# Kernel tuning notes

Measured on AMD Instinct MI355X. Metric: run time of the kernel, lower is better.

Reference implementation:

```python
import jax, jax.numpy as jnp
import numpy as np

TAU = 0.07
EPS_NORM = 1e-8


def setup_inputs() -> dict:
    key = jax.random.key(0)
    k1, k2 = jax.random.split(key)
    N, D = 8192, 128
    feats = jax.random.normal(k1, (N, D), dtype=jnp.float32)
    labels = jax.random.randint(k2, (N,), 0, 512, dtype=jnp.int64)
    return {"feats": feats, "labels": labels}


def _l2n(x, eps=EPS_NORM):
    # F.normalize: x / max(||x||_2, eps)
    n = jnp.sqrt(jnp.sum(x * x, axis=-1, keepdims=True))
    return x / jnp.maximum(n, eps)


def reference(feats, labels):
    N = feats.shape[0]
    f = _l2n(feats)
    sim = (f @ f.T) / TAU                       # [N, N]
    eye = jnp.eye(N, dtype=sim.dtype)
    logits = sim - eye * 1e9                    # suppress self-similarity
    pos_mask = (labels[:, None] == labels[None, :]) & (~jnp.eye(N, dtype=bool))
    exp_logits = jnp.exp(logits)                # [N, N]
    numer = jnp.sum(exp_logits * pos_mask, axis=1)
    denom = jnp.maximum(jnp.sum(exp_logits, axis=1), 1e-8)
    valid = jnp.sum(pos_mask, axis=1) > 0
    loss = -jnp.log((numer + 1e-12) / denom)    # [N]
    n_valid = jnp.sum(valid)
    mean_loss = jnp.sum(jnp.where(valid, loss, 0.0)) / jnp.maximum(n_valid, 1)
    return jnp.where(n_valid > 0, mean_loss, 0.0)
```

## Files before the change

### kernel.cpp

```cpp
#include <hip/hip_runtime.h>
#include <hip/hip_bf16.h>

#define N_ROWS 8192
#define DIM 128
#define IBLK 128

#define SQRT_SC 4.539816f
#define LN2F 0.6931471805599453f

typedef __attribute__((ext_vector_type(8))) short bf16x8;
typedef __attribute__((ext_vector_type(4))) float f32x4;

__global__ __launch_bounds__(256) void normalize_kernel(
    const float* __restrict__ feats, __hip_bfloat16* __restrict__ nf) {
  int wid = threadIdx.x >> 6;
  int lane = threadIdx.x & 63;
  int row = blockIdx.x * 4 + wid;
  const float* rp = feats + (size_t)row * DIM;
  float2 v = *reinterpret_cast<const float2*>(rp + lane * 2);
  float ss = v.x * v.x + v.y * v.y;
  #pragma unroll
  for (int m = 1; m < 64; m <<= 1) ss += __shfl_xor(ss, m, 64);
  float scale = SQRT_SC / fmaxf(sqrtf(ss), 1e-8f);
  __hip_bfloat162 h2;
  h2.x = __float2bfloat16(v.x * scale);
  h2.y = __float2bfloat16(v.y * scale);
  *reinterpret_cast<__hip_bfloat162*>(nf + (size_t)row * DIM + lane * 2) = h2;
}

__global__ __launch_bounds__(256) void supcon_main(
    const __hip_bfloat16* __restrict__ nf, const int* __restrict__ labels,
    float* __restrict__ denomP, float* __restrict__ numerP, int jrange) {
  const ushort* F = reinterpret_cast<const ushort*>(nf);
  int lane = threadIdx.x & 63;
  int wid = threadIdx.x >> 6;
  int col = lane & 15;
  int kg = lane >> 4;
  int ibase = blockIdx.x * IBLK + wid * 32;
  int jbase = blockIdx.y * jrange;

  bf16x8 a[2][4];
  int labi[2][4];
  #pragma unroll
  for (int it = 0; it < 2; ++it) {
    const ushort* ap = F + (size_t)(ibase + it * 16 + col) * DIM + kg * 8;
    #pragma unroll
    for (int c = 0; c < 4; ++c)
      a[it][c] = *reinterpret_cast<const bf16x8*>(ap + c * 32);
    #pragma unroll
    for (int r = 0; r < 4; ++r)
      labi[it][r] = labels[ibase + it * 16 + kg * 4 + r];
  }
  float denom[2][4] = {}, numer[2][4] = {};

  const ushort* bp = F + (size_t)(jbase + col) * DIM + kg * 8;
  const int* lp = labels + jbase + col;
  int ntiles = jrange >> 4;
  for (int jt = 0; jt < ntiles; ++jt) {
    int jb = jbase + (jt << 4);
    int labj = *lp;
    bf16x8 b[4];
    #pragma unroll
    for (int c = 0; c < 4; ++c)
      b[c] = *reinterpret_cast<const bf16x8*>(bp + c * 32);
    f32x4 d[2];
    #pragma unroll
    for (int it = 0; it < 2; ++it) {
      f32x4 acc = {0.f, 0.f, 0.f, 0.f};
      #pragma unroll
      for (int c = 0; c < 4; ++c)
        acc = __builtin_amdgcn_mfma_f32_16x16x32_bf16(a[it][c], b[c], acc,
                                                      0, 0, 0);
      d[it] = acc;
    }
    if (jb + 16 > ibase && jb < ibase + 32) {
      int gj = jb + col;
      #pragma unroll
      for (int it = 0; it < 2; ++it)
        #pragma unroll
        for (int r = 0; r < 4; ++r) {
          float e = __builtin_amdgcn_exp2f(d[it][r]);
          if (ibase + it * 16 + kg * 4 + r == gj) e = 0.f;
          denom[it][r] += e;
          numer[it][r] += (labi[it][r] == labj) ? e : 0.f;
        }
    } else {
      #pragma unroll
      for (int it = 0; it < 2; ++it)
        #pragma unroll
        for (int r = 0; r < 4; ++r) {
          float e = __builtin_amdgcn_exp2f(d[it][r]);
          denom[it][r] += e;
          numer[it][r] += (labi[it][r] == labj) ? e : 0.f;
        }
    }
    bp += (size_t)16 * DIM;
    lp += 16;
  }

  #pragma unroll
  for (int m = 1; m < 16; m <<= 1)
    #pragma unroll
    for (int it = 0; it < 2; ++it)
      #pragma unroll
      for (int r = 0; r < 4; ++r) {
        denom[it][r] += __shfl_xor(denom[it][r], m, 64);
        numer[it][r] += __shfl_xor(numer[it][r], m, 64);
      }
  if (col == 0) {
    size_t s = blockIdx.y;
    #pragma unroll
    for (int it = 0; it < 2; ++it)
      #pragma unroll
      for (int r = 0; r < 4; ++r) {
        size_t idx = s * N_ROWS + (ibase + it * 16 + kg * 4 + r);
        denomP[idx] = denom[it][r];
        numerP[idx] = numer[it][r];
      }
  }
}

__global__ __launch_bounds__(256) void finalize1(
    const float* __restrict__ denomP, const float* __restrict__ numerP,
    const int* __restrict__ labels, float* __restrict__ blkP, int jsplit) {
  __shared__ int hist[512];
  int tid = threadIdx.x;
  for (int i = tid; i < 512; i += 256) hist[i] = 0;
  __syncthreads();
  for (int i = tid; i < N_ROWS; i += 256) atomicAdd(&hist[labels[i]], 1);
  __syncthreads();

  int row = blockIdx.x * 256 + tid;
  float den = 0.f, num = 0.f;
  for (int s = 0; s < jsplit; ++s) {
    den += denomP[(size_t)s * N_ROWS + row];
    num += numerP[(size_t)s * N_ROWS + row];
  }
  bool valid = (hist[labels[row]] - 1) > 0;
  float loss = LN2F * (__builtin_amdgcn_logf(fmaxf(den, 1e-8f)) -
                       __builtin_amdgcn_logf(num + 1e-12f));
  float ls = valid ? loss : 0.f;
  float lc = valid ? 1.f : 0.f;
  #pragma unroll
  for (int m = 1; m < 64; m <<= 1) {
    ls += __shfl_xor(ls, m, 64);
    lc += __shfl_xor(lc, m, 64);
  }
  __shared__ float ss[4], sc[4];
  int wid = tid >> 6, lane = tid & 63;
  if (lane == 0) { ss[wid] = ls; sc[wid] = lc; }
  __syncthreads();
  if (tid == 0) {
    blkP[blockIdx.x * 2] = ss[0] + ss[1] + ss[2] + ss[3];
    blkP[blockIdx.x * 2 + 1] = sc[0] + sc[1] + sc[2] + sc[3];
  }
}

__global__ __launch_bounds__(64) void finalize2(const float* __restrict__ blkP,
                                                float* __restrict__ out) {
  int lane = threadIdx.x;
  float s = (lane < 32) ? blkP[lane * 2] : 0.f;
  float c = (lane < 32) ? blkP[lane * 2 + 1] : 0.f;
  #pragma unroll
  for (int m = 1; m < 64; m <<= 1) {
    s += __shfl_xor(s, m, 64);
    c += __shfl_xor(c, m, 64);
  }
  if (lane == 0) out[0] = (c > 0.f) ? s / c : 0.f;
}

extern "C" void kernel_launch(void* const* d_in, const int* in_sizes, int n_in,
                              void* d_out, int out_size, void* d_ws,
                              size_t ws_size, hipStream_t stream) {
  const float* feats = (const float*)d_in[0];
  const int* labels = (const int*)d_in[1];
  float* out = (float*)d_out;

  __hip_bfloat16* nf = (__hip_bfloat16*)d_ws;
  size_t nf_bytes = (size_t)N_ROWS * DIM * sizeof(__hip_bfloat16);

  int jsplit = 16;
  while (jsplit > 1 &&
         ws_size < nf_bytes + ((size_t)jsplit * N_ROWS * 2 + 64) * sizeof(float))
    jsplit >>= 1;
  int jrange = N_ROWS / jsplit;

  float* denomP = (float*)((char*)d_ws + nf_bytes);
  float* numerP = denomP + (size_t)jsplit * N_ROWS;
  float* blkP = numerP + (size_t)jsplit * N_ROWS;

  normalize_kernel<<<N_ROWS / 4, 256, 0, stream>>>(feats, nf);
  supcon_main<<<dim3(N_ROWS / IBLK, jsplit), 256, 0, stream>>>(
      nf, labels, denomP, numerP, jrange);
  finalize1<<<32, 256, 0, stream>>>(denomP, numerP, labels, blkP, jsplit);
  finalize2<<<1, 64, 0, stream>>>(blkP, out);
}
```

Before: 135.6 us.

## Stage B tiles in LDS with async double buffering and larger per-wave i-tiles

```diff
diff --git a/kernel.cpp b/kernel.cpp
--- a/kernel.cpp
+++ b/kernel.cpp
@@ -3,13 +3,17 @@
 
 #define N_ROWS 8192
 #define DIM 128
-#define IBLK 128
+#define WI 64
+#define IBLK 256
+#define BJ 64
 
 #define SQRT_SC 4.539816f
 #define LN2F 0.6931471805599453f
 
 typedef __attribute__((ext_vector_type(8))) short bf16x8;
 typedef __attribute__((ext_vector_type(4))) float f32x4;
+typedef __attribute__((address_space(3))) unsigned int as3_u32;
+typedef const __attribute__((address_space(1))) unsigned int as1_u32;
 
 __global__ __launch_bounds__(256) void normalize_kernel(
     const float* __restrict__ feats, __hip_bfloat16* __restrict__ nf) {
@@ -28,80 +32,111 @@
   *reinterpret_cast<__hip_bfloat162*>(nf + (size_t)row * DIM + lane * 2) = h2;
 }
 
-__global__ __launch_bounds__(256) void supcon_main(
+__global__ __launch_bounds__(256, 2) void supcon_main(
     const __hip_bfloat16* __restrict__ nf, const int* __restrict__ labels,
     float* __restrict__ denomP, float* __restrict__ numerP, int jrange) {
+  __shared__ ushort Bs[2][BJ * DIM];
   const ushort* F = reinterpret_cast<const ushort*>(nf);
-  int lane = threadIdx.x & 63;
-  int wid = threadIdx.x >> 6;
-  int col = lane & 15;
-  int kg = lane >> 4;
-  int ibase = blockIdx.x * IBLK + wid * 32;
-  int jbase = blockIdx.y * jrange;
-
-  bf16x8 a[2][4];
-  int labi[2][4];
-  #pragma unroll
-  for (int it = 0; it < 2; ++it) {
-    const ushort* ap = F + (size_t)(ibase + it * 16 + col) * DIM + kg * 8;
+  const int lane = threadIdx.x & 63;
+  const int wid = threadIdx.x >> 6;
+  const int col = lane & 15;
+  const int kg = lane >> 4;
+  const int wibase = blockIdx.x * IBLK + wid * WI;
+  const int jbase = blockIdx.y * jrange;
+
+  bf16x8 a[4][4];
+  int labi[4][4];
+  #pragma unroll
+  for (int it = 0; it < 4; ++it) {
+    const ushort* ap = F + (size_t)(wibase + it * 16 + col) * DIM + kg * 8;
     #pragma unroll
     for (int c = 0; c < 4; ++c)
       a[it][c] = *reinterpret_cast<const bf16x8*>(ap + c * 32);
     #pragma unroll
     for (int r = 0; r < 4; ++r)
-      labi[it][r] = labels[ibase + it * 16 + kg * 4 + r];
-  }
-  float denom[2][4] = {}, numer[2][4] = {};
-
-  const ushort* bp = F + (size_t)(jbase + col) * DIM + kg * 8;
-  const int* lp = labels + jbase + col;
-  int ntiles = jrange >> 4;
-  for (int jt = 0; jt < ntiles; ++jt) {
-    int jb = jbase + (jt << 4);
-    int labj = *lp;
-    bf16x8 b[4];
-    #pragma unroll
-    for (int c = 0; c < 4; ++c)
-      b[c] = *reinterpret_cast<const bf16x8*>(bp + c * 32);
-    f32x4 d[2];
-    #pragma unroll
-    for (int it = 0; it < 2; ++it) {
-      f32x4 acc = {0.f, 0.f, 0.f, 0.f};
-      #pragma unroll
-      for (int c = 0; c < 4; ++c)
-        acc = __builtin_amdgcn_mfma_f32_16x16x32_bf16(a[it][c], b[c], acc,
-                                                      0, 0, 0);
-      d[it] = acc;
+      labi[it][r] = labels[wibase + it * 16 + kg * 4 + r];
+  }
+  float denom[4][4] = {}, numer[4][4] = {};
+
+  const int srow = lane >> 4;
+  const int schunk = lane & 15;
+
+  const int nst = jrange / BJ;
+
+#define STAGE(BUFI, JB)                                                        \
+  {                                                                            \
+    _Pragma("unroll") for (int i = 0; i < 4; ++i) {                            \
+      int r = wid * 16 + i * 4 + srow;                                         \
+      int gc = schunk ^ (r & 15);                                              \
+      const ushort* gp = F + (((size_t)((JB) + r)) << 7) + (gc << 3);          \
+      __builtin_amdgcn_global_load_lds(                                        \
+          (as1_u32*)gp, (as3_u32*)(&Bs[BUFI][(wid * 16 + i * 4) * DIM]), 16,   \
+          0, 0);                                                               \
+    }                                                                          \
+  }
+
+  STAGE(0, jbase)
+  __syncthreads();
+
+  for (int t = 0; t < nst; ++t) {
+    const int cur = t & 1;
+    const int jb0 = jbase + t * BJ;
+    if (t + 1 < nst) STAGE(cur ^ 1, jb0 + BJ)
+
+    int labj[4];
+    #pragma unroll
+    for (int sub = 0; sub < 4; ++sub) labj[sub] = labels[jb0 + sub * 16 + col];
+
+    #pragma unroll
+    for (int sub = 0; sub < 4; ++sub) {
+      const int jb = jb0 + sub * 16;
+      const ushort* bs = &Bs[cur][sub * 16 * DIM];
+      bf16x8 b[4];
+      #pragma unroll
+      for (int c = 0; c < 4; ++c) {
+        int sc = (c * 4 + kg) ^ col;
+        b[c] = *reinterpret_cast<const bf16x8*>(bs + col * DIM + sc * 8);
+      }
+      f32x4 d[4];
+      #pragma unroll
+      for (int it = 0; it < 4; ++it) {
+        f32x4 acc = {0.f, 0.f, 0.f, 0.f};
+        #pragma unroll
+        for (int c = 0; c < 4; ++c)
+          acc = __builtin_amdgcn_mfma_f32_16x16x32_bf16(a[it][c], b[c], acc,
+                                                        0, 0, 0);
+        d[it] = acc;
+      }
+      if (jb < wibase + WI && jb + 16 > wibase) {
+        int gj = jb + col;
+        #pragma unroll
+        for (int it = 0; it < 4; ++it)
+          #pragma unroll
+          for (int r = 0; r < 4; ++r) {
+            float e = __builtin_amdgcn_exp2f(d[it][r]);
+            if (wibase + it * 16 + kg * 4 + r == gj) e = 0.f;
+            denom[it][r] += e;
+            numer[it][r] += (labi[it][r] == labj[sub]) ? e : 0.f;
+          }
+      } else {
+        #pragma unroll
+        for (int it = 0; it < 4; ++it)
+          #pragma unroll
+          for (int r = 0; r < 4; ++r) {
+            float e = __builtin_amdgcn_exp2f(d[it][r]);
+            denom[it][r] += e;
+            numer[it][r] += (labi[it][r] == labj[sub]) ? e : 0.f;
+          }
+      }
     }
-    if (jb + 16 > ibase && jb < ibase + 32) {
-      int gj = jb + col;
-      #pragma unroll
-      for (int it = 0; it < 2; ++it)
-        #pragma unroll
-        for (int r = 0; r < 4; ++r) {
-          float e = __builtin_amdgcn_exp2f(d[it][r]);
-          if (ibase + it * 16 + kg * 4 + r == gj) e = 0.f;
-          denom[it][r] += e;
-          numer[it][r] += (labi[it][r] == labj) ? e : 0.f;
-        }
-    } else {
-      #pragma unroll
-      for (int it = 0; it < 2; ++it)
-        #pragma unroll
-        for (int r = 0; r < 4; ++r) {
-          float e = __builtin_amdgcn_exp2f(d[it][r]);
-          denom[it][r] += e;
-          numer[it][r] += (labi[it][r] == labj) ? e : 0.f;
-        }
-    }
-    bp += (size_t)16 * DIM;
-    lp += 16;
-  }
+    __syncthreads();
+  }
+#undef STAGE
 
   #pragma unroll
   for (int m = 1; m < 16; m <<= 1)
     #pragma unroll
-    for (int it = 0; it < 2; ++it)
+    for (int it = 0; it < 4; ++it)
       #pragma unroll
       for (int r = 0; r < 4; ++r) {
         denom[it][r] += __shfl_xor(denom[it][r], m, 64);
@@ -110,10 +145,10 @@
   if (col == 0) {
     size_t s = blockIdx.y;
     #pragma unroll
-    for (int it = 0; it < 2; ++it)
+    for (int it = 0; it < 4; ++it)
       #pragma unroll
       for (int r = 0; r < 4; ++r) {
-        size_t idx = s * N_ROWS + (ibase + it * 16 + kg * 4 + r);
+        size_t idx = s * N_ROWS + (wibase + it * 16 + kg * 4 + r);
         denomP[idx] = denom[it][r];
         numerP[idx] = numer[it][r];
       }
@@ -146,13 +181,13 @@
     ls += __shfl_xor(ls, m, 64);
     lc += __shfl_xor(lc, m, 64);
   }
-  __shared__ float ss[4], sc[4];
+  __shared__ float ss[4], sc2[4];
   int wid = tid >> 6, lane = tid & 63;
-  if (lane == 0) { ss[wid] = ls; sc[wid] = lc; }
+  if (lane == 0) { ss[wid] = ls; sc2[wid] = lc; }
   __syncthreads();
   if (tid == 0) {
     blkP[blockIdx.x * 2] = ss[0] + ss[1] + ss[2] + ss[3];
-    blkP[blockIdx.x * 2 + 1] = sc[0] + sc[1] + sc[2] + sc[3];
+    blkP[blockIdx.x * 2 + 1] = sc2[0] + sc2[1] + sc2[2] + sc2[3];
   }
 }
 
```

After: 115.1 us. 15.2% less time.
